# Kernel optimization log

Measured on AMD Instinct MI355X. Metric: run time of the kernel, lower is better.

The kernel has to match this reference:

```python
import jax, jax.numpy as jnp
import numpy as np

NQ = 4          # n_qubits == hidden_dim (required for gate broadcasting)
D = 256         # embed_dim
H = 4           # num_heads
HD = D // H     # head_dim
V = 32000       # vocab
TAG = 64        # tagset_size
B, T = 16, 512


def _apply_rx(state, theta, wire):
    # state: (B, 2,2,2,2) complex64; theta: (B,) angles. RX = [[c,-is],[-is,c]], c=cos(t/2)
    half = theta * 0.5
    c = jnp.cos(half).reshape(-1, 1, 1, 1).astype(state.real.dtype)
    s = jnp.sin(half).reshape(-1, 1, 1, 1).astype(state.real.dtype)
    st = jnp.moveaxis(state, wire + 1, 1)
    a, b = st[:, 0], st[:, 1]
    st2 = jnp.stack([c * a - 1j * s * b, c * b - 1j * s * a], axis=1)
    return jnp.moveaxis(st2, 1, wire + 1)


def _apply_cnot(state, ctrl, tgt):
    st = jnp.moveaxis(state, (ctrl + 1, tgt + 1), (1, 2))
    st2 = jnp.stack([st[:, 0], st[:, 1, ::-1]], axis=1)  # flip target when ctrl=1
    return jnp.moveaxis(st2, (1, 2), (ctrl + 1, tgt + 1))


def _qlayer(angles, thetas):
    # angles: (B, NQ) data-encoding RX angles; thetas: (NQ,) trainable RX angles
    bsz = angles.shape[0]
    state = jnp.zeros((bsz,) + (2,) * NQ, jnp.complex64)
    state = state.at[(slice(None),) + (0,) * NQ].set(1.0)
    for w in range(NQ):
        state = _apply_rx(state, angles[:, w], w)
    for w in range(NQ):
        state = _apply_rx(state, jnp.broadcast_to(thetas[w], (bsz,)), w)
    for w in range(NQ - 1):
        state = _apply_cnot(state, w, w + 1)
    state = _apply_cnot(state, NQ - 1, 0)
    probs = state.real ** 2 + state.imag ** 2
    pm = jnp.array([1.0, -1.0], probs.dtype)
    outs = [
        jnp.sum(probs * pm.reshape((1,) + tuple(2 if i == w else 1 for i in range(NQ))),
                axis=tuple(range(1, NQ + 1)))
        for w in range(NQ)
    ]
    return jnp.stack(outs, axis=-1)  # (B, NQ) PauliZ expectations


def _forward(sentence, emb, Wq, bq, Wk, bk, Wv, bv, Wo, bo,
             Wf, bf, thf, Wi, bi, thi, Wg, bg, thg, Wo2, bo2, tho, Wt, bt):
    x = emb[sentence]  # (B, T, D)
    Bc, Tc, _ = x.shape
    # multi-head self-attention
    q = (x @ Wq.T + bq).reshape(Bc, Tc, H, HD).transpose(0, 2, 1, 3)
    k = (x @ Wk.T + bk).reshape(Bc, Tc, H, HD).transpose(0, 2, 1, 3)
    v = (x @ Wv.T + bv).reshape(Bc, Tc, H, HD).transpose(0, 2, 1, 3)
    scores = jnp.einsum('bhqd,bhkd->bhqk', q, k) / (HD ** 0.5)
    attn = jax.nn.softmax(scores, axis=-1)
    o = jnp.einsum('bhqk,bhkd->bhqd', attn, v).transpose(0, 2, 1, 3).reshape(Bc, Tc, D)
    attn_out = o @ Wo.T + bo  # (B, T, D)

    # quantum LSTM over time via scan
    def step(carry, x_t):
        hx, cx = carry  # (B, NQ) each
        comb = jnp.concatenate([x_t, hx], axis=-1)  # (B, D+NQ)
        f = jax.nn.sigmoid(_qlayer(comb @ Wf.T + bf, thf))
        i = jax.nn.sigmoid(_qlayer(comb @ Wi.T + bi, thi))
        g = jnp.tanh(_qlayer(comb @ Wg.T + bg, thg))
        oo = jax.nn.sigmoid(_qlayer(comb @ Wo2.T + bo2, tho))
        cx = f * cx + i * g
        hx = oo * jnp.tanh(cx)
        return (hx, cx), hx

    h0 = jnp.zeros((Bc, NQ), x.dtype)
    _, hs = jax.lax.scan(step, (h0, h0), attn_out.transpose(1, 0, 2))  # (T, B, NQ)
    lstm_out = hs.transpose(1, 0, 2)  # (B, T, NQ)
    logits = lstm_out @ Wt.T + bt
    return jax.nn.log_softmax(logits, axis=-1)


def setup_inputs() -> dict:
    key = jax.random.key(0)
    ks = jax.random.split(key, 24)
    n = lambda k, shp, sc=0.02: (jax.random.normal(k, shp, jnp.float32) * sc)
    DQ = D + NQ
    return {
        'sentence': jax.random.randint(ks[0], (B, T), 0, V),
        'emb': n(ks[1], (V, D), 1.0),
        'Wq': n(ks[2], (D, D)), 'bq': jnp.zeros((D,), jnp.float32),
        'Wk': n(ks[3], (D, D)), 'bk': jnp.zeros((D,), jnp.float32),
        'Wv': n(ks[4], (D, D)), 'bv': jnp.zeros((D,), jnp.float32),
        'Wo': n(ks[5], (D, D)), 'bo': jnp.zeros((D,), jnp.float32),
        'Wf': n(ks[6], (NQ, DQ), 0.05), 'bf': jnp.zeros((NQ,), jnp.float32),
        'thf': jax.random.uniform(ks[7], (NQ,), jnp.float32, 0.0, 2 * np.pi),
        'Wi': n(ks[8], (NQ, DQ), 0.05), 'bi': jnp.zeros((NQ,), jnp.float32),
        'thi': jax.random.uniform(ks[9], (NQ,), jnp.float32, 0.0, 2 * np.pi),
        'Wg': n(ks[10], (NQ, DQ), 0.05), 'bg': jnp.zeros((NQ,), jnp.float32),
        'thg': jax.random.uniform(ks[11], (NQ,), jnp.float32, 0.0, 2 * np.pi),
        'Wo2': n(ks[12], (NQ, DQ), 0.05), 'bo2': jnp.zeros((NQ,), jnp.float32),
        'tho': jax.random.uniform(ks[13], (NQ,), jnp.float32, 0.0, 2 * np.pi),
        'Wt': n(ks[14], (TAG, NQ), 0.1), 'bt': jnp.zeros((TAG,), jnp.float32),
    }


def reference(sentence, emb, Wq, bq, Wk, bk, Wv, bv, Wo, bo,
              Wf, bf, thf, Wi, bi, thi, Wg, bg, thg, Wo2, bo2, tho, Wt, bt):
    return _forward(sentence, emb, Wq, bq, Wk, bk, Wv, bv, Wo, bo,
                    Wf, bf, thf, Wi, bi, thi, Wg, bg, thg, Wo2, bo2, tho, Wt, bt)
```

## Files before the change

kernel.cpp:

```cpp
#include <hip/hip_runtime.h>
#include <hip/hip_bf16.h>

#define NB 16
#define NT 512
#define ND 256
#define NH 4
#define NHD 64
#define NTAG 64

typedef short bf16x8 __attribute__((ext_vector_type(8)));
typedef float f32x4 __attribute__((ext_vector_type(4)));
union LdsVec { uint4 u; bf16x8 v; };

#define INV2PI 0.15915494309189535f

__device__ __forceinline__ float ldf(const void* p, int isbf, long i) {
  return isbf ? __bfloat162float(((const __hip_bfloat16*)p)[i])
              : ((const float*)p)[i];
}
__device__ __forceinline__ unsigned short bfbits(float f) {
  __hip_bfloat16 h = __float2bfloat16(f);
  union { __hip_bfloat16 h; unsigned short s; } u{h};
  return u.s;
}
__device__ __forceinline__ unsigned int pack2(float a, float b) {
  return ((unsigned int)bfbits(b) << 16) | bfbits(a);
}

template <int CTRL>
__device__ __forceinline__ float dppf(float v) {
  return __int_as_float(
      __builtin_amdgcn_update_dpp(0, __float_as_int(v), CTRL, 0xF, 0xF, false));
}

__device__ __forceinline__ float frcp(float x) {
#if __has_builtin(__builtin_amdgcn_rcpf)
  return __builtin_amdgcn_rcpf(x);
#else
  float r; asm("v_rcp_f32 %0, %1" : "=v"(r) : "v"(x)); return r;
#endif
}
__device__ __forceinline__ float fexp2(float x) {
#if __has_builtin(__builtin_amdgcn_exp2f)
  return __builtin_amdgcn_exp2f(x);
#else
  float r; asm("v_exp_f32 %0, %1" : "=v"(r) : "v"(x)); return r;
#endif
}
__device__ __forceinline__ float fcosr(float x) {
#if __has_builtin(__builtin_amdgcn_cosf)
  return __builtin_amdgcn_cosf(x);
#else
  float r; asm("v_cos_f32 %0, %1" : "=v"(r) : "v"(x)); return r;
#endif
}

__device__ __forceinline__ int detect_isbf(const void* buf, int nview) {
  __shared__ int s_big;
  if (threadIdx.x == 0) s_big = 0;
  __syncthreads();
  const __hip_bfloat16* p = (const __hip_bfloat16*)buf;
  int big = 0;
  for (int i = threadIdx.x; i < nview; i += blockDim.x) {
    float v = __bfloat162float(p[i]);
    if (fabsf(v) > 1e4f) big = 1;
  }
  if (big) atomicOr(&s_big, 1);
  __syncthreads();
  return s_big ? 0 : 1;
}

#define AST 264
#define BST 40
__global__ __launch_bounds__(256) void k_qkvc(
    const int* __restrict__ sent, const void* emb,
    const void* Wq, const void* Wk, const void* Wv,
    const void* bq, const void* bk, const void* bv,
    const void* Wo, const void* bo,
    const void* Wf, const void* Wi, const void* Wg, const void* Wo2,
    const void* bF, const void* bI, const void* bG, const void* bO,
    const void* thF, const void* thI, const void* thG, const void* thO,
    __hip_bfloat16* Qbf, __hip_bfloat16* Kbf, __hip_bfloat16* Vtbf,
    __hip_bfloat16* __restrict__ Mbf, float* __restrict__ cvb) {
  __shared__ __align__(16) unsigned short SH[64 * AST + 4 * 64 * BST];
  unsigned short* AS = SH;
  unsigned short* BS = SH + 64 * AST;
  int z = blockIdx.z;
  int tid = threadIdx.x;

  if (z == 3) {
    if (blockIdx.x >= 4) return;
    float (*WGs)[256] = (float(*)[256])SH;
    int isbf = detect_isbf(Wo, 4096);
    for (int e = tid; e < 4096; e += 256) {
      int oi = e >> 8, j = e & 255;
      int gate = oi >> 2, w = oi & 3;
      const void* Ws = (gate == 0) ? Wf : (gate == 1) ? Wi : (gate == 2) ? Wg : Wo2;
      WGs[oi][j] = ldf(Ws, isbf, (long)w * 260 + j);
    }
    __syncthreads();
    if (tid < 64) {
      int d = blockIdx.x * 64 + tid;
      float m[16];
#pragma unroll
      for (int oi = 0; oi < 16; ++oi) m[oi] = 0.f;
#pragma unroll 4
      for (int j = 0; j < 256; ++j) {
        float wo = ldf(Wo, isbf, (long)j * 256 + d);
#pragma unroll
        for (int oi = 0; oi < 16; ++oi) m[oi] += WGs[oi][j] * wo;
      }
#pragma unroll
      for (int oi = 0; oi < 16; ++oi)
        Mbf[oi * 256 + d] = __float2bfloat16(m[oi]);
    }
    if (blockIdx.x == 0 && tid < 16) {
      int gate = tid >> 2, w = tid & 3;
      float cc = 0.f;
      for (int j = 0; j < 256; ++j) cc += WGs[tid][j] * ldf(bo, isbf, j);
      const void* bsel = (gate == 0) ? bF : (gate == 1) ? bI : (gate == 2) ? bG : bO;
      const void* tsel = (gate == 0) ? thF : (gate == 1) ? thI : (gate == 2) ? thG : thO;
      cvb[tid] = (cc + ldf(bsel, isbf, w) + ldf(tsel, isbf, w)) * INV2PI;
    }
    return;
  }

  const void* W = (z == 0) ? Wq : (z == 1) ? Wk : Wv;
  const void* Bb = (z == 0) ? bq : (z == 1) ? bk : bv;
  __hip_bfloat16* O = (z == 0) ? Qbf : (z == 1) ? Kbf : Vtbf;
  int isbf = detect_isbf(W, 1024);

  int rowbase = blockIdx.x * 64;
  int wave = tid >> 6, lane = tid & 63;
  int li = lane & 15, quad = lane >> 4;
  int colbase = wave * 64;
  unsigned short* Bw = &BS[wave * 64 * BST];

  const float* Wf32 = (const float*)W;
  const __hip_bfloat16* Wb16 = (const __hip_bfloat16*)W;
  long wrow = (long)(colbase + lane) * 256;

  float4 bf[8];
  uint4 bb4[4];
  if (isbf) {
#pragma unroll
    for (int j = 0; j < 4; ++j) bb4[j] = *(const uint4*)&Wb16[wrow + j * 8];
  } else {
#pragma unroll
    for (int j = 0; j < 8; ++j) bf[j] = *(const float4*)&Wf32[wrow + j * 4];
  }

  {
    int srow = tid >> 2;
    int sc = (tid & 3) * 64;
    long tok = (long)sent[rowbase + srow];
    if (isbf) {
      const __hip_bfloat16* eb = (const __hip_bfloat16*)emb + tok * 256 + sc;
#pragma unroll
      for (int j = 0; j < 8; ++j)
        *(uint4*)&AS[srow * AST + sc + j * 8] = *(const uint4*)&eb[j * 8];
    } else {
      const float* ef = (const float*)emb + tok * 256 + sc;
#pragma unroll
      for (int j = 0; j < 8; ++j) {
        float4 lo = *(const float4*)&ef[j * 8];
        float4 hi = *(const float4*)&ef[j * 8 + 4];
        uint4 pk;
        pk.x = pack2(lo.x, lo.y); pk.y = pack2(lo.z, lo.w);
        pk.z = pack2(hi.x, hi.y); pk.w = pack2(hi.z, hi.w);
        *(uint4*)&AS[srow * AST + sc + j * 8] = pk;
      }
    }
  }
  __syncthreads();

  f32x4 acc[4][4];
#pragma unroll
  for (int mt = 0; mt < 4; ++mt)
#pragma unroll
    for (int nt = 0; nt < 4; ++nt) acc[mt][nt] = (f32x4){0.f, 0.f, 0.f, 0.f};

#pragma unroll
  for (int k0 = 0; k0 < 256; k0 += 32) {
    if (isbf) {
#pragma unroll
      for (int j = 0; j < 4; ++j)
        *(uint4*)&Bw[lane * BST + j * 8] = bb4[j];
    } else {
#pragma unroll
      for (int j = 0; j < 4; ++j) {
        uint4 pk;
        pk.x = pack2(bf[2 * j].x, bf[2 * j].y);
        pk.y = pack2(bf[2 * j].z, bf[2 * j].w);
        pk.z = pack2(bf[2 * j + 1].x, bf[2 * j + 1].y);
        pk.w = pack2(bf[2 * j + 1].z, bf[2 * j + 1].w);
        *(uint4*)&Bw[lane * BST + j * 8] = pk;
      }
    }
    if (k0 < 224) {
      if (isbf) {
#pragma unroll
        for (int j = 0; j < 4; ++j)
          bb4[j] = *(const uint4*)&Wb16[wrow + k0 + 32 + j * 8];
      } else {
#pragma unroll
        for (int j = 0; j < 8; ++j)
          bf[j] = *(const float4*)&Wf32[wrow + k0 + 32 + j * 4];
      }
    }
    LdsVec a[4], b[4];
#pragma unroll
    for (int mt = 0; mt < 4; ++mt)
      a[mt].u = *(const uint4*)&AS[(mt * 16 + li) * AST + k0 + quad * 8];
#pragma unroll
    for (int nt = 0; nt < 4; ++nt)
      b[nt].u = *(const uint4*)&Bw[(nt * 16 + li) * BST + quad * 8];
#pragma unroll
    for (int mt = 0; mt < 4; ++mt)
#pragma unroll
      for (int nt = 0; nt < 4; ++nt)
        acc[mt][nt] = __builtin_amdgcn_mfma_f32_16x16x32_bf16(
            a[mt].v, b[nt].v, acc[mt][nt], 0, 0, 0);
  }

  __syncthreads();
  if (z == 2) {
#pragma unroll
    for (int nt = 0; nt < 4; ++nt) {
      int col = colbase + nt * 16 + li;
      float bias = ldf(Bb, isbf, col);
#pragma unroll
      for (int mt = 0; mt < 4; ++mt)
#pragma unroll
        for (int reg = 0; reg < 4; ++reg)
          SH[col * 72 + mt * 16 + quad * 4 + reg] =
              bfbits(acc[mt][nt][reg] + bias);
    }
  } else {
#pragma unroll
    for (int nt = 0; nt < 4; ++nt) {
      int col = colbase + nt * 16 + li;
      float bias = ldf(Bb, isbf, col);
#pragma unroll
      for (int mt = 0; mt < 4; ++mt)
#pragma unroll
        for (int reg = 0; reg < 4; ++reg)
          SH[(mt * 16 + quad * 4 + reg) * AST + col] =
              bfbits(acc[mt][nt][reg] + bias);
    }
  }
  __syncthreads();
  int bb2 = blockIdx.x >> 3, ttb = (blockIdx.x & 7) * 64;
  if (z == 2) {
#pragma unroll
    for (int j = 0; j < 8; ++j) {
      int e = tid + j * 256;
      int hdcol = e >> 3, c8 = (e & 7) * 8;
      uint4 v = *(const uint4*)&SH[hdcol * 72 + c8];
      *(uint4*)((__hip_bfloat16*)O +
                ((long)(bb2 * 4 + (hdcol >> 6)) * 64 + (hdcol & 63)) * 512 +
                ttb + c8) = v;
    }
  } else {
#pragma unroll
    for (int j = 0; j < 8; ++j) {
      int e = tid + j * 256;
      int row = e >> 5, c8e = (e & 31) * 8;
      int h = c8e >> 6, hd = c8e & 63;
      uint4 v = *(const uint4*)&SH[row * AST + c8e];
      *(uint4*)((__hip_bfloat16*)O +
                ((long)(bb2 * 4 + h) * 512 + ttb + row) * 64 + hd) = v;
    }
  }
}

#define LSTR 72
__global__ __launch_bounds__(256) void k_attn(const __hip_bfloat16* __restrict__ Qg,
                                              const __hip_bfloat16* __restrict__ Kg,
                                              const __hip_bfloat16* __restrict__ Vtg,
                                              const __hip_bfloat16* __restrict__ Mbf,
                                              float* __restrict__ P) {
  __shared__ __align__(16) unsigned short Qs[64 * LSTR];
  __shared__ __align__(16) unsigned short Ks[2][64 * LSTR];
  __shared__ __align__(16) unsigned short Vts[2][64 * LSTR];
  __shared__ __align__(16) unsigned short Ps[64 * LSTR];
  int tid = threadIdx.x;
  int bh = blockIdx.x, qt = blockIdx.y;
  int wave = tid >> 6, lane = tid & 63, li = lane & 15, quad = lane >> 4;

  int r0 = tid >> 3, c80 = (tid & 7) * 8;
  int idx1 = tid + 256;
  int r1 = idx1 >> 3, c81 = (idx1 & 7) * 8;

  const __hip_bfloat16* Qb = Qg + ((long)bh * 512 + qt * 64) * 64;
  *(uint4*)&Qs[r0 * LSTR + c80] = *(const uint4*)&Qb[(long)r0 * 64 + c80];
  *(uint4*)&Qs[r1 * LSTR + c81] = *(const uint4*)&Qb[(long)r1 * 64 + c81];

  uint4 kr0, kr1, vr0, vr1;
  {
    const __hip_bfloat16* Kb = Kg + ((long)bh * 512 + 0 * 64) * 64;
    kr0 = *(const uint4*)&Kb[(long)r0 * 64 + c80];
    kr1 = *(const uint4*)&Kb[(long)r1 * 64 + c81];
    vr0 = *(const uint4*)&Vtg[((long)bh * 64 + r0) * 512 + 0 * 64 + c80];
    vr1 = *(const uint4*)&Vtg[((long)bh * 64 + r1) * 512 + 0 * 64 + c81];
  }
  *(uint4*)&Ks[0][r0 * LSTR + c80] = kr0;
  *(uint4*)&Ks[0][r1 * LSTR + c81] = kr1;
  *(uint4*)&Vts[0][r0 * LSTR + c80] = vr0;
  *(uint4*)&Vts[0][r1 * LSTR + c81] = vr1;
  __syncthreads();

  f32x4 accO[4];
  float mrow[4], lrow[4];
#pragma unroll
  for (int i = 0; i < 4; ++i) {
    accO[i] = (f32x4){0.f, 0.f, 0.f, 0.f};
    mrow[i] = -1e30f; lrow[i] = 0.f;
  }

#pragma unroll 1
  for (int kt = 0; kt < 8; ++kt) {
    int cur = kt & 1;
    if (kt < 7) {
      const __hip_bfloat16* Kb = Kg + ((long)bh * 512 + (kt + 1) * 64) * 64;
      kr0 = *(const uint4*)&Kb[(long)r0 * 64 + c80];
      kr1 = *(const uint4*)&Kb[(long)r1 * 64 + c81];
      vr0 = *(const uint4*)&Vtg[((long)bh * 64 + r0) * 512 + (kt + 1) * 64 + c80];
      vr1 = *(const uint4*)&Vtg[((long)bh * 64 + r1) * 512 + (kt + 1) * 64 + c81];
    }

    f32x4 s[4];
#pragma unroll
    for (int nb = 0; nb < 4; ++nb) s[nb] = (f32x4){0.f, 0.f, 0.f, 0.f};
#pragma unroll
    for (int nb = 0; nb < 4; ++nb)
#pragma unroll
      for (int kc = 0; kc < 2; ++kc) {
        LdsVec a, b;
        a.u = *(const uint4*)&Qs[(wave * 16 + li) * LSTR + kc * 32 + quad * 8];
        b.u = *(const uint4*)&Ks[cur][(nb * 16 + li) * LSTR + kc * 32 + quad * 8];
        s[nb] = __builtin_amdgcn_mfma_f32_16x16x32_bf16(a.v, b.v, s[nb], 0, 0, 0);
      }
#pragma unroll
    for (int nb = 0; nb < 4; ++nb) s[nb] *= 0.125f;

#pragma unroll
    for (int reg = 0; reg < 4; ++reg) {
      float rm = fmaxf(fmaxf(s[0][reg], s[1][reg]), fmaxf(s[2][reg], s[3][reg]));
      rm = fmaxf(rm, __shfl_xor(rm, 1));
      rm = fmaxf(rm, __shfl_xor(rm, 2));
      rm = fmaxf(rm, __shfl_xor(rm, 4));
      rm = fmaxf(rm, __shfl_xor(rm, 8));
      float mnew = fmaxf(mrow[reg], rm);
      float alpha = __expf(mrow[reg] - mnew);
      mrow[reg] = mnew;
      float psum = 0.f;
#pragma unroll
      for (int nb = 0; nb < 4; ++nb) {
        float p = __expf(s[nb][reg] - mnew);
        psum += p;
        Ps[(wave * 16 + quad * 4 + reg) * LSTR + nb * 16 + li] = bfbits(p);
      }
      psum += __shfl_xor(psum, 1);
      psum += __shfl_xor(psum, 2);
      psum += __shfl_xor(psum, 4);
      psum += __shfl_xor(psum, 8);
      lrow[reg] = lrow[reg] * alpha + psum;
#pragma unroll
      for (int db = 0; db < 4; ++db) accO[db][reg] *= alpha;
    }

#pragma unroll
    for (int db = 0; db < 4; ++db)
#pragma unroll
      for (int kc = 0; kc < 2; ++kc) {
        LdsVec a, b;
        a.u = *(const uint4*)&Ps[(wave * 16 + li) * LSTR + kc * 32 + quad * 8];
        b.u = *(const uint4*)&Vts[cur][(db * 16 + li) * LSTR + kc * 32 + quad * 8];
        accO[db] = __builtin_amdgcn_mfma_f32_16x16x32_bf16(a.v, b.v, accO[db], 0, 0, 0);
      }

    if (kt < 7) {
      int nxt = cur ^ 1;
      *(uint4*)&Ks[nxt][r0 * LSTR + c80] = kr0;
      *(uint4*)&Ks[nxt][r1 * LSTR + c81] = kr1;
      *(uint4*)&Vts[nxt][r0 * LSTR + c80] = vr0;
      *(uint4*)&Vts[nxt][r1 * LSTR + c81] = vr1;
    }
    __syncthreads();
  }

  int batch = bh >> 2, head = bh & 3;
  if (tid < 128) {
    int r = tid >> 3, c8 = (tid & 7) * 8;
    *(uint4*)&Qs[r * LSTR + c8] = *(const uint4*)&Mbf[r * 256 + head * 64 + c8];
  }
#pragma unroll
  for (int reg = 0; reg < 4; ++reg) {
    float inv = 1.f / lrow[reg];
#pragma unroll
    for (int db = 0; db < 4; ++db)
      Ps[(wave * 16 + quad * 4 + reg) * LSTR + db * 16 + li] =
          bfbits(accO[db][reg] * inv);
  }
  __syncthreads();
  f32x4 pacc = (f32x4){0.f, 0.f, 0.f, 0.f};
#pragma unroll
  for (int kc = 0; kc < 2; ++kc) {
    LdsVec a, b;
    a.u = *(const uint4*)&Ps[(wave * 16 + li) * LSTR + kc * 32 + quad * 8];
    b.u = *(const uint4*)&Qs[li * LSTR + kc * 32 + quad * 8];
    pacc = __builtin_amdgcn_mfma_f32_16x16x32_bf16(a.v, b.v, pacc, 0, 0, 0);
  }
  int pblk = batch >> 2, brow = (batch & 3) * 16 + li;
  long off = ((long)((head * 4 + pblk) * 64 + brow)) * 512 +
             qt * 64 + wave * 16 + quad * 4;
  float4 st;
  st.x = pacc[0] * INV2PI; st.y = pacc[1] * INV2PI;
  st.z = pacc[2] * INV2PI; st.w = pacc[3] * INV2PI;
  *(float4*)&P[off] = st;
}

#define SWEEPS 4
#define CHUNK 16
#define NCH 32

template <bool DIRB>
__device__ __forceinline__ void scan_sweeps(
    const float* __restrict__ Pb, float cvv,
    int c, int G, int w,
    float rr0, float rr1, float rr2, float rr3,
    float kk, float e1, float mkm1,
    int s0, int s1, int s2, int s3,
    float (*bH)[NCH + 1][4], float (*bC)[NCH + 1][4],
    float* __restrict__ hsb) {
  float pcv[CHUNK];
#pragma unroll
  for (int j4 = 0; j4 < CHUNK / 4; ++j4) {
    float4 a = *(const float4*)&Pb[0 * 131072 + c * 16 + j4 * 4];
    float4 b = *(const float4*)&Pb[1 * 131072 + c * 16 + j4 * 4];
    float4 d = *(const float4*)&Pb[2 * 131072 + c * 16 + j4 * 4];
    float4 e = *(const float4*)&Pb[3 * 131072 + c * 16 + j4 * 4];
    pcv[j4 * 4 + 0] = cvv + a.x + b.x + d.x + e.x;
    pcv[j4 * 4 + 1] = cvv + a.y + b.y + d.y + e.y;
    pcv[j4 * 4 + 2] = cvv + a.z + b.z + d.z + e.z;
    pcv[j4 * 4 + 3] = cvv + a.w + b.w + d.w + e.w;
  }

#pragma unroll 1
  for (int s = 0; s < SWEEPS; ++s) {
    int rd = s & 1, wr = rd ^ 1;
    float h0 = bH[rd][c][0], h1 = bH[rd][c][1];
    float h2 = bH[rd][c][2], h3 = bH[rd][c][3];
    float cx = bC[rd][c][w];
    float hx = 0.f;
#pragma unroll
    for (int u = 0; u < CHUNK; ++u) {
      float pc = pcv[u];
      float d01 = __builtin_fmaf(rr1, h1, __builtin_fmaf(rr0, h0, pc));
      float d23 = __builtin_fmaf(rr3, h3, rr2 * h2);
      float a = d01 + d23;
      float cth = fcosr(a);
      float c0 = dppf<0x00>(cth), c1 = dppf<0x55>(cth);
      float c2 = dppf<0xAA>(cth), c3 = dppf<0xFF>(cth);
      float p01 = c0 * c1, z23 = c2 * c3;
      float v = (w == 0) ? c1 * z23 : (w == 1) ? p01
              : (w == 2) ? p01 * c2 : p01 * z23;
      float val = __builtin_fmaf(kk, frcp(1.f + fexp2(e1 * v)), mkm1);
      float ra = dppf<0x124>(val);
      float rb = dppf<0x128>(val);
      float rc = dppf<0x12C>(val);
      float rot1 = DIRB ? ra : rc;
      float rot3 = DIRB ? rc : ra;
      float f = (s0 == 0) ? val : (s0 == 1) ? rot1 : (s0 == 2) ? rb : rot3;
      float i = (s1 == 0) ? val : (s1 == 1) ? rot1 : (s1 == 2) ? rb : rot3;
      float g = (s2 == 0) ? val : (s2 == 1) ? rot1 : (s2 == 2) ? rb : rot3;
      float o = (s3 == 0) ? val : (s3 == 1) ? rot1 : (s3 == 2) ? rb : rot3;
      cx = __builtin_fmaf(f, cx, i * g);
      float rt = frcp(1.f + fexp2(-2.88539008f * cx));
      hx = __builtin_fmaf(o + o, rt, -o);
      h0 = dppf<0x00>(hx); h1 = dppf<0x55>(hx);
      h2 = dppf<0xAA>(hx); h3 = dppf<0xFF>(hx);
      if (G == 0) hsb[(c * CHUNK + u) * 4 + w] = hx;
    }
    if (G == 0) {
      bH[wr][c + 1][w] = hx;
      bC[wr][c + 1][w] = cx;
    }
    __syncthreads();
  }
}

__global__ __launch_bounds__(512) void k_scanf(const float* __restrict__ P,
                                               const float* __restrict__ cvb,
                                               const void* Wf, const void* Wi,
                                               const void* Wg, const void* Wo2,
                                               const void* Wt, const void* Bt,
                                               void* outp) {
  __shared__ float bH[2][NCH + 1][4];
  __shared__ float bC[2][NCH + 1][4];
  __shared__ __align__(16) float hsb[512 * 4];
  __shared__ float sWt[256];
  __shared__ float sBt[64];
  int tid = threadIdx.x;
  int b = blockIdx.x;
  int c = tid >> 4;
  int l16 = tid & 15;
  int G = l16 >> 2, w = l16 & 3;
  int lane = tid & 63;

  if (tid < 2 * (NCH + 1) * 4) {
    ((float*)bH)[tid] = 0.f;
    ((float*)bC)[tid] = 0.f;
  }

  const __hip_bfloat16* pw = (const __hip_bfloat16*)Wf;
  int big = 0;
  for (int i = lane; i < 1040; i += 64) {
    float v = __bfloat162float(pw[i]);
    if (fabsf(v) > 1e4f) big = 1;
  }
  int isbf = (__ballot(big) == 0ULL) ? 1 : 0;

  if (tid < 256) sWt[tid] = ldf(Wt, isbf, tid);
  else if (tid < 320) sBt[tid - 256] = ldf(Bt, isbf, tid - 256);

  int got = __builtin_amdgcn_update_dpp(0, lane, 0x124, 0xF, 0xF, false);
  int dir = __shfl((got == 9) ? 1 : 0, 5);
  const void* Wsel = (G == 0) ? Wf : (G == 1) ? Wi : (G == 2) ? Wg : Wo2;
  float rr0 = ldf(Wsel, isbf, (long)w * 260 + 256 + 0) * INV2PI;
  float rr1 = ldf(Wsel, isbf, (long)w * 260 + 256 + 1) * INV2PI;
  float rr2 = ldf(Wsel, isbf, (long)w * 260 + 256 + 2) * INV2PI;
  float rr3 = ldf(Wsel, isbf, (long)w * 260 + 256 + 3) * INV2PI;
  float kk = (G == 2) ? 2.f : 1.f;
  float e1 = -kk * 1.44269504f;
  float mkm1 = 1.f - kk;
  int s0 = (0 - G) & 3, s1 = (1 - G) & 3, s2 = (2 - G) & 3, s3 = (3 - G) & 3;

  const float* Pb = P + ((long)(b >> 2) * 64 + (b & 3) * 16 + l16) * 512;
  float cvv = cvb[l16];
  __syncthreads();

  if (dir)
    scan_sweeps<true>(Pb, cvv, c, G, w, rr0, rr1, rr2, rr3,
                      kk, e1, mkm1, s0, s1, s2, s3, bH, bC, hsb);
  else
    scan_sweeps<false>(Pb, cvv, c, G, w, rr0, rr1, rr2, rr3,
                       kk, e1, mkm1, s0, s1, s2, s3, bH, bC, hsb);

  float h0 = hsb[tid * 4 + 0], h1 = hsb[tid * 4 + 1];
  float h2 = hsb[tid * 4 + 2], h3 = hsb[tid * 4 + 3];
  float lg[64];
  float mx = -1e30f;
#pragma unroll
  for (int j = 0; j < 64; ++j) {
    float v = sBt[j]
            + h0 * sWt[j * 4 + 0] + h1 * sWt[j * 4 + 1]
            + h2 * sWt[j * 4 + 2] + h3 * sWt[j * 4 + 3];
    lg[j] = v;
    mx = fmaxf(mx, v);
  }
  float ssum = 0.f;
#pragma unroll
  for (int j = 0; j < 64; ++j) ssum += __expf(lg[j] - mx);
  float sub = mx + __logf(ssum);
  long rbase = ((long)b * 512 + tid) * 64;
  if (isbf) {
    __hip_bfloat16* ob = (__hip_bfloat16*)outp;
#pragma unroll
    for (int j0 = 0; j0 < 8; ++j0) {
      uint4 pk;
      pk.x = pack2(lg[j0 * 8 + 0] - sub, lg[j0 * 8 + 1] - sub);
      pk.y = pack2(lg[j0 * 8 + 2] - sub, lg[j0 * 8 + 3] - sub);
      pk.z = pack2(lg[j0 * 8 + 4] - sub, lg[j0 * 8 + 5] - sub);
      pk.w = pack2(lg[j0 * 8 + 6] - sub, lg[j0 * 8 + 7] - sub);
      *(uint4*)(ob + rbase + j0 * 8) = pk;
    }
  } else {
    float* of = (float*)outp;
#pragma unroll
    for (int j0 = 0; j0 < 16; ++j0) {
      float4 v4;
      v4.x = lg[j0 * 4 + 0] - sub; v4.y = lg[j0 * 4 + 1] - sub;
      v4.z = lg[j0 * 4 + 2] - sub; v4.w = lg[j0 * 4 + 3] - sub;
      *(float4*)(of + rbase + j0 * 4) = v4;
    }
  }
}

extern "C" void kernel_launch(void* const* d_in, const int* in_sizes, int n_in,
                              void* d_out, int out_size, void* d_ws, size_t ws_size,
                              hipStream_t stream) {
  const int* sent = (const int*)d_in[0];
  const void* emb = d_in[1];
  const void* Wq = d_in[2];  const void* bq = d_in[3];
  const void* Wk = d_in[4];  const void* bk = d_in[5];
  const void* Wv = d_in[6];  const void* bv = d_in[7];
  const void* Wo = d_in[8];  const void* bo = d_in[9];
  const void* Wf = d_in[10]; const void* bF = d_in[11]; const void* thF = d_in[12];
  const void* Wi = d_in[13]; const void* bI = d_in[14]; const void* thI = d_in[15];
  const void* Wg = d_in[16]; const void* bG = d_in[17]; const void* thG = d_in[18];
  const void* Wo2 = d_in[19]; const void* bO = d_in[20]; const void* thO = d_in[21];
  const void* Wt = d_in[22]; const void* Bt = d_in[23];

  float* base = (float*)((char*)d_ws + 256);
  __hip_bfloat16* Mbf = (__hip_bfloat16*)base;
  float* cvb = base + 2048;
  __hip_bfloat16* Qbf  = (__hip_bfloat16*)(base + 4096);
  __hip_bfloat16* Kbf  = (__hip_bfloat16*)(base + 4096 + 1048576);
  __hip_bfloat16* Vtbf = (__hip_bfloat16*)(base + 4096 + 2097152);
  float* Pp = base + 4096 + 3145728;

  dim3 gq(128, 1, 4);
  k_qkvc<<<gq, 256, 0, stream>>>(sent, emb, Wq, Wk, Wv, bq, bk, bv, Wo, bo,
                                 Wf, Wi, Wg, Wo2, bF, bI, bG, bO,
                                 thF, thI, thG, thO, Qbf, Kbf, Vtbf, Mbf, cvb);
  dim3 ga(64, 8, 1);
  k_attn<<<ga, 256, 0, stream>>>(Qbf, Kbf, Vtbf, Mbf, Pp);
  k_scanf<<<16, 512, 0, stream>>>(Pp, cvb, Wf, Wi, Wg, Wo2, Wt, Bt, d_out);
}
```

Measured before the change: 229.6 us.

## Compute Q, K and V in one block per row tile reusing staged embeddings

Each QKV block now loops over the three weight matrices, so the gathered embedding tile is loaded into shared memory once instead of three times. The grid shrinks from 512 blocks to 132, with the last 4 blocks handling the Wo-fold precompute. A separate output staging region is added to shared memory so the A tile survives across the three projections, and the first chunk of the next weight matrix is prefetched during the last k-step. The cost is fewer blocks on a large GPU, which reduces parallelism, plus more LDS per block.

```diff
diff --git a/kernel.cpp b/kernel.cpp
--- a/kernel.cpp
+++ b/kernel.cpp
@@ -82,14 +82,14 @@
     const void* thF, const void* thI, const void* thG, const void* thO,
     __hip_bfloat16* Qbf, __hip_bfloat16* Kbf, __hip_bfloat16* Vtbf,
     __hip_bfloat16* __restrict__ Mbf, float* __restrict__ cvb) {
-  __shared__ __align__(16) unsigned short SH[64 * AST + 4 * 64 * BST];
+  __shared__ __align__(16) unsigned short SH[64 * AST + 4 * 64 * BST + 256 * 72];
   unsigned short* AS = SH;
   unsigned short* BS = SH + 64 * AST;
-  int z = blockIdx.z;
+  unsigned short* CS = SH + 64 * AST + 4 * 64 * BST;
   int tid = threadIdx.x;
 
-  if (z == 3) {
-    if (blockIdx.x >= 4) return;
+  if (blockIdx.x >= 128) {
+    int cb = blockIdx.x - 128;
     float (*WGs)[256] = (float(*)[256])SH;
     int isbf = detect_isbf(Wo, 4096);
     for (int e = tid; e < 4096; e += 256) {
@@ -100,7 +100,7 @@
     }
     __syncthreads();
     if (tid < 64) {
-      int d = blockIdx.x * 64 + tid;
+      int d = cb * 64 + tid;
       float m[16];
 #pragma unroll
       for (int oi = 0; oi < 16; ++oi) m[oi] = 0.f;
@@ -114,7 +114,7 @@
       for (int oi = 0; oi < 16; ++oi)
         Mbf[oi * 256 + d] = __float2bfloat16(m[oi]);
     }
-    if (blockIdx.x == 0 && tid < 16) {
+    if (cb == 0 && tid < 16) {
       int gate = tid >> 2, w = tid & 3;
       float cc = 0.f;
       for (int j = 0; j < 256; ++j) cc += WGs[tid][j] * ldf(bo, isbf, j);
@@ -125,30 +125,28 @@
     return;
   }
 
-  const void* W = (z == 0) ? Wq : (z == 1) ? Wk : Wv;
-  const void* Bb = (z == 0) ? bq : (z == 1) ? bk : bv;
-  __hip_bfloat16* O = (z == 0) ? Qbf : (z == 1) ? Kbf : Vtbf;
-  int isbf = detect_isbf(W, 1024);
+  int isbf = detect_isbf(Wq, 1024);
 
   int rowbase = blockIdx.x * 64;
   int wave = tid >> 6, lane = tid & 63;
   int li = lane & 15, quad = lane >> 4;
   int colbase = wave * 64;
   unsigned short* Bw = &BS[wave * 64 * BST];
-
-  const float* Wf32 = (const float*)W;
-  const __hip_bfloat16* Wb16 = (const __hip_bfloat16*)W;
   long wrow = (long)(colbase + lane) * 256;
 
   float4 bf[8];
   uint4 bb4[4];
-  if (isbf) {
-#pragma unroll
-    for (int j = 0; j < 4; ++j) bb4[j] = *(const uint4*)&Wb16[wrow + j * 8];
-  } else {
-#pragma unroll
-    for (int j = 0; j < 8; ++j) bf[j] = *(const float4*)&Wf32[wrow + j * 4];
-  }
+#define LOADB(WP, OFS)                                                  \
+  if (isbf) {                                                           \
+    const __hip_bfloat16* wp_ = (const __hip_bfloat16*)(WP);            \
+    _Pragma("unroll") for (int j_ = 0; j_ < 4; ++j_)                    \
+      bb4[j_] = *(const uint4*)&wp_[wrow + (OFS) + j_ * 8];             \
+  } else {                                                              \
+    const float* wp_ = (const float*)(WP);                              \
+    _Pragma("unroll") for (int j_ = 0; j_ < 8; ++j_)                    \
+      bf[j_] = *(const float4*)&wp_[wrow + (OFS) + j_ * 4];             \
+  }
+  LOADB(Wq, 0)
 
   {
     int srow = tid >> 2;
@@ -174,102 +172,105 @@
   }
   __syncthreads();
 
-  f32x4 acc[4][4];
-#pragma unroll
-  for (int mt = 0; mt < 4; ++mt)
-#pragma unroll
-    for (int nt = 0; nt < 4; ++nt) acc[mt][nt] = (f32x4){0.f, 0.f, 0.f, 0.f};
-
-#pragma unroll
-  for (int k0 = 0; k0 < 256; k0 += 32) {
-    if (isbf) {
-#pragma unroll
-      for (int j = 0; j < 4; ++j)
-        *(uint4*)&Bw[lane * BST + j * 8] = bb4[j];
+  int bb2 = blockIdx.x >> 3, ttb = (blockIdx.x & 7) * 64;
+
+#pragma unroll 1
+  for (int wsel = 0; wsel < 3; ++wsel) {
+    const void* W = (wsel == 0) ? Wq : (wsel == 1) ? Wk : Wv;
+    const void* Wnxt = (wsel == 0) ? Wk : Wv;
+    const void* Bb = (wsel == 0) ? bq : (wsel == 1) ? bk : bv;
+    __hip_bfloat16* O = (wsel == 0) ? Qbf : (wsel == 1) ? Kbf : Vtbf;
+
+    f32x4 acc[4][4];
+#pragma unroll
+    for (int mt = 0; mt < 4; ++mt)
+#pragma unroll
+      for (int nt = 0; nt < 4; ++nt) acc[mt][nt] = (f32x4){0.f, 0.f, 0.f, 0.f};
+
+#pragma unroll
+    for (int k0 = 0; k0 < 256; k0 += 32) {
+      if (isbf) {
+#pragma unroll
+        for (int j = 0; j < 4; ++j)
+          *(uint4*)&Bw[lane * BST + j * 8] = bb4[j];
+      } else {
+#pragma unroll
+        for (int j = 0; j < 4; ++j) {
+          uint4 pk;
+          pk.x = pack2(bf[2 * j].x, bf[2 * j].y);
+          pk.y = pack2(bf[2 * j].z, bf[2 * j].w);
+          pk.z = pack2(bf[2 * j + 1].x, bf[2 * j + 1].y);
+          pk.w = pack2(bf[2 * j + 1].z, bf[2 * j + 1].w);
+          *(uint4*)&Bw[lane * BST + j * 8] = pk;
+        }
+      }
+      if (k0 < 224) {
+        LOADB(W, k0 + 32)
+      } else if (wsel < 2) {
+        LOADB(Wnxt, 0)
+      }
+      LdsVec a[4], b[4];
+#pragma unroll
+      for (int mt = 0; mt < 4; ++mt)
+        a[mt].u = *(const uint4*)&AS[(mt * 16 + li) * AST + k0 + quad * 8];
+#pragma unroll
+      for (int nt = 0; nt < 4; ++nt)
+        b[nt].u = *(const uint4*)&Bw[(nt * 16 + li) * BST + quad * 8];
+#pragma unroll
+      for (int mt = 0; mt < 4; ++mt)
+#pragma unroll
+        for (int nt = 0; nt < 4; ++nt)
+          acc[mt][nt] = __builtin_amdgcn_mfma_f32_16x16x32_bf16(
+              a[mt].v, b[nt].v, acc[mt][nt], 0, 0, 0);
+    }
+
+    __syncthreads();
+    if (wsel == 2) {
+#pragma unroll
+      for (int nt = 0; nt < 4; ++nt) {
+        int col = colbase + nt * 16 + li;
+        float bias = ldf(Bb, isbf, col);
+#pragma unroll
+        for (int mt = 0; mt < 4; ++mt)
+#pragma unroll
+          for (int reg = 0; reg < 4; ++reg)
+            CS[col * 72 + mt * 16 + quad * 4 + reg] =
+                bfbits(acc[mt][nt][reg] + bias);
+      }
     } else {
 #pragma unroll
-      for (int j = 0; j < 4; ++j) {
-        uint4 pk;
-        pk.x = pack2(bf[2 * j].x, bf[2 * j].y);
-        pk.y = pack2(bf[2 * j].z, bf[2 * j].w);
-        pk.z = pack2(bf[2 * j + 1].x, bf[2 * j + 1].y);
-        pk.w = pack2(bf[2 * j + 1].z, bf[2 * j + 1].w);
-        *(uint4*)&Bw[lane * BST + j * 8] = pk;
-      }
-    }
-    if (k0 < 224) {
-      if (isbf) {
-#pragma unroll
-        for (int j = 0; j < 4; ++j)
-          bb4[j] = *(const uint4*)&Wb16[wrow + k0 + 32 + j * 8];
-      } else {
-#pragma unroll
-        for (int j = 0; j < 8; ++j)
-          bf[j] = *(const float4*)&Wf32[wrow + k0 + 32 + j * 4];
-      }
-    }
-    LdsVec a[4], b[4];
-#pragma unroll
-    for (int mt = 0; mt < 4; ++mt)
-      a[mt].u = *(const uint4*)&AS[(mt * 16 + li) * AST + k0 + quad * 8];
-#pragma unroll
-    for (int nt = 0; nt < 4; ++nt)
-      b[nt].u = *(const uint4*)&Bw[(nt * 16 + li) * BST + quad * 8];
-#pragma unroll
-    for (int mt = 0; mt < 4; ++mt)
-#pragma unroll
-      for (int nt = 0; nt < 4; ++nt)
-        acc[mt][nt] = __builtin_amdgcn_mfma_f32_16x16x32_bf16(
-            a[mt].v, b[nt].v, acc[mt][nt], 0, 0, 0);
-  }
-
-  __syncthreads();
-  if (z == 2) {
-#pragma unroll
-    for (int nt = 0; nt < 4; ++nt) {
-      int col = colbase + nt * 16 + li;
-      float bias = ldf(Bb, isbf, col);
-#pragma unroll
-      for (int mt = 0; mt < 4; ++mt)
-#pragma unroll
-        for (int reg = 0; reg < 4; ++reg)
-          SH[col * 72 + mt * 16 + quad * 4 + reg] =
-              bfbits(acc[mt][nt][reg] + bias);
-    }
-  } else {
-#pragma unroll
-    for (int nt = 0; nt < 4; ++nt) {
-      int col = colbase + nt * 16 + li;
-      float bias = ldf(Bb, isbf, col);
-#pragma unroll
-      for (int mt = 0; mt < 4; ++mt)
-#pragma unroll
-        for (int reg = 0; reg < 4; ++reg)
-          SH[(mt * 16 + quad * 4 + reg) * AST + col] =
-              bfbits(acc[mt][nt][reg] + bias);
-    }
-  }
-  __syncthreads();
-  int bb2 = blockIdx.x >> 3, ttb = (blockIdx.x & 7) * 64;
-  if (z == 2) {
-#pragma unroll
-    for (int j = 0; j < 8; ++j) {
-      int e = tid + j * 256;
-      int hdcol = e >> 3, c8 = (e & 7) * 8;
-      uint4 v = *(const uint4*)&SH[hdcol * 72 + c8];
-      *(uint4*)((__hip_bfloat16*)O +
-                ((long)(bb2 * 4 + (hdcol >> 6)) * 64 + (hdcol & 63)) * 512 +
-                ttb + c8) = v;
-    }
-  } else {
-#pragma unroll
-    for (int j = 0; j < 8; ++j) {
-      int e = tid + j * 256;
-      int row = e >> 5, c8e = (e & 31) * 8;
-      int h = c8e >> 6, hd = c8e & 63;
-      uint4 v = *(const uint4*)&SH[row * AST + c8e];
-      *(uint4*)((__hip_bfloat16*)O +
-                ((long)(bb2 * 4 + h) * 512 + ttb + row) * 64 + hd) = v;
+      for (int nt = 0; nt < 4; ++nt) {
+        int col = colbase + nt * 16 + li;
+        float bias = ldf(Bb, isbf, col);
+#pragma unroll
+        for (int mt = 0; mt < 4; ++mt)
+#pragma unroll
+          for (int reg = 0; reg < 4; ++reg)
+            CS[(mt * 16 + quad * 4 + reg) * AST + col] =
+                bfbits(acc[mt][nt][reg] + bias);
+      }
+    }
+    __syncthreads();
+    if (wsel == 2) {
+#pragma unroll
+      for (int j = 0; j < 8; ++j) {
+        int e = tid + j * 256;
+        int hdcol = e >> 3, c8 = (e & 7) * 8;
+        uint4 v = *(const uint4*)&CS[hdcol * 72 + c8];
+        *(uint4*)((__hip_bfloat16*)O +
+                  ((long)(bb2 * 4 + (hdcol >> 6)) * 64 + (hdcol & 63)) * 512 +
+                  ttb + c8) = v;
+      }
+    } else {
+#pragma unroll
+      for (int j = 0; j < 8; ++j) {
+        int e = tid + j * 256;
+        int row = e >> 5, c8e = (e & 31) * 8;
+        int h = c8e >> 6, hd = c8e & 63;
+        uint4 v = *(const uint4*)&CS[row * AST + c8e];
+        *(uint4*)((__hip_bfloat16*)O +
+                  ((long)(bb2 * 4 + h) * 512 + ttb + row) * 64 + hd) = v;
+      }
     }
   }
 }
@@ -611,10 +612,9 @@
   __hip_bfloat16* Vtbf = (__hip_bfloat16*)(base + 4096 + 2097152);
   float* Pp = base + 4096 + 3145728;
 
-  dim3 gq(128, 1, 4);
-  k_qkvc<<<gq, 256, 0, stream>>>(sent, emb, Wq, Wk, Wv, bq, bk, bv, Wo, bo,
-                                 Wf, Wi, Wg, Wo2, bF, bI, bG, bO,
-                                 thF, thI, thG, thO, Qbf, Kbf, Vtbf, Mbf, cvb);
+  k_qkvc<<<132, 256, 0, stream>>>(sent, emb, Wq, Wk, Wv, bq, bk, bv, Wo, bo,
+                                  Wf, Wi, Wg, Wo2, bF, bI, bG, bO,
+                                  thF, thI, thG, thO, Qbf, Kbf, Vtbf, Mbf, cvb);
   dim3 ga(64, 8, 1);
   k_attn<<<ga, 256, 0, stream>>>(Qbf, Kbf, Vtbf, Mbf, Pp);
   k_scanf<<<16, 512, 0, stream>>>(Pp, cvb, Wf, Wi, Wg, Wo2, Wt, Bt, d_out);
```

Measured after the change: 223.6 us. -2.6%, faster.
